# Performance work log

Hardware: AMD Instinct MI355X
Metric: run time of the kernel (lower is better)

## Reference

```python
import jax, jax.numpy as jnp
import numpy as np

B = 32768
N_SPARSE = 26
N_DENSE = 13
VOCAB = 10000
E = 64
H = 2
L = 3
DH = E // H
DNN_IN = N_DENSE + N_SPARSE * E  # 1677
H1, H2 = 256, 128


def setup_inputs() -> dict:
    key = jax.random.key(0)
    ks = jax.random.split(key, 12)
    sparse_idx = jax.random.randint(ks[0], (B, N_SPARSE), 0, VOCAB, dtype=jnp.int32)
    dense = jax.random.uniform(ks[1], (B, N_DENSE), dtype=jnp.float32)
    X = jnp.concatenate([sparse_idx.astype(jnp.float32), dense], axis=1)  # [B,39]
    emb_tables = jax.random.normal(ks[2], (N_SPARSE, VOCAB, E), dtype=jnp.float32)
    Wq = jax.random.normal(ks[3], (L, E, E), dtype=jnp.float32) * 0.05
    Wk = jax.random.normal(ks[4], (L, E, E), dtype=jnp.float32) * 0.05
    Wv = jax.random.normal(ks[5], (L, E, E), dtype=jnp.float32) * 0.05
    Wres = jax.random.normal(ks[6], (L, E, E), dtype=jnp.float32) * 0.05
    dnn_W1 = jax.random.normal(ks[7], (DNN_IN, H1), dtype=jnp.float32) * 1e-4
    dnn_b1 = jnp.zeros((H1,), dtype=jnp.float32)
    dnn_W2 = jax.random.normal(ks[8], (H1, H2), dtype=jnp.float32) * 1e-4
    dnn_b2 = jnp.zeros((H2,), dtype=jnp.float32)
    out_W = jax.random.normal(ks[9], (N_SPARSE * E + H2, 1), dtype=jnp.float32) * 1e-5
    lin_W = jax.random.normal(ks[10], (N_SPARSE + N_DENSE, 1), dtype=jnp.float32) * 1e-5
    lin_b = jnp.zeros((1,), dtype=jnp.float32)
    return {"X": X, "sparse_idx": sparse_idx, "emb_tables": emb_tables,
            "Wq": Wq, "Wk": Wk, "Wv": Wv, "Wres": Wres,
            "dnn_W1": dnn_W1, "dnn_b1": dnn_b1, "dnn_W2": dnn_W2, "dnn_b2": dnn_b2,
            "out_W": out_W, "lin_W": lin_W, "lin_b": lin_b}


def _split_heads(x):
    # torch.stack(torch.split(x, DH, dim=2)) -> [H, B, F, DH]
    b, f, _ = x.shape
    return jnp.moveaxis(x.reshape(b, f, H, DH), 2, 0)


def _interacting_layer(att, wq, wk, wv, wres):
    # att: [B, F, E]
    q = _split_heads(jnp.einsum('bfe,eo->bfo', att, wq))  # [H,B,F,DH]
    k = _split_heads(jnp.einsum('bfe,eo->bfo', att, wk))
    v = _split_heads(jnp.einsum('bfe,eo->bfo', att, wv))
    scores = jnp.einsum('hbik,hbjk->hbij', q, k)           # [H,B,F,F] (no scaling: default scaling=False)
    attn = jax.nn.softmax(scores, axis=-1)
    out = jnp.einsum('hbij,hbjd->hbid', attn, v)           # [H,B,F,DH]
    b, f = att.shape[0], att.shape[1]
    out = jnp.moveaxis(out, 0, 2).reshape(b, f, E)         # cat heads along last dim
    out = out + jnp.einsum('bfe,eo->bfo', att, wres)       # residual (use_res=True)
    return jax.nn.relu(out)


def reference(X, sparse_idx, emb_tables, Wq, Wk, Wv, Wres,
              dnn_W1, dnn_b1, dnn_W2, dnn_b2, out_W, lin_W, lin_b):
    # linear logit tower (dropout in eval mode -> identity)
    logit = jax.nn.relu(X @ lin_W + lin_b)                 # [B,1]
    # embedding gather: table f indexed by sparse_idx[:,f]
    emb = emb_tables[jnp.arange(N_SPARSE), sparse_idx]     # [B, F, E]
    att = emb
    for l in range(L):
        att = _interacting_layer(att, Wq[l], Wk[l], Wv[l], Wres[l])
    att_flat = att.reshape(att.shape[0], -1)               # [B, F*E]
    sparse_flat = emb.reshape(emb.shape[0], -1)            # [B, F*E]
    dense_input = X[:, N_SPARSE:]                          # [B, 13]
    dnn_in = jnp.concatenate([dense_input, sparse_flat], axis=1)
    h = jax.nn.relu(dnn_in @ dnn_W1 + dnn_b1)
    h = jax.nn.relu(h @ dnn_W2 + dnn_b2)
    stack = jnp.concatenate([att_flat, h], axis=-1)
    logit = logit + stack @ out_W
    return jax.nn.sigmoid(logit)
```

## Files before the change

kernel.cpp:

```cpp
#include <hip/hip_runtime.h>
#include <math.h>

#define BATCH 32768
#define NSP 26
#define NDN 13
#define VOC 10000
#define EDIM 64
#define NLAY 3
#define HID1 256
#define HID2 128
#define XW 39
#define KCH 27

typedef __fp16   fp16x2 __attribute__((ext_vector_type(2)));
typedef _Float16 half8  __attribute__((ext_vector_type(8)));
typedef float float4v   __attribute__((ext_vector_type(4)));

__device__ __forceinline__ unsigned pkh(float lo, float hi) {
    fp16x2 h = __builtin_amdgcn_cvt_pkrtz(lo, hi);
    return __builtin_bit_cast(unsigned, h);
}
__device__ __forceinline__ unsigned short f2h(float f) {
    return __builtin_bit_cast(unsigned short, (_Float16)f);
}
__device__ __forceinline__ float h2f(unsigned short h) {
    return (float)__builtin_bit_cast(_Float16, h);
}
__device__ __forceinline__ uint2 pkC(float4v c) {
    uint2 r; r.x = pkh(c[0], c[1]); r.y = pkh(c[2], c[3]); return r;
}
__device__ __forceinline__ void st4(unsigned short* p, float4v v) {
    *(uint2*)p = pkC(v);
}
__device__ __forceinline__ half8 cat(uint2 a, uint2 b) {
    union { unsigned u[4]; half8 h; } r;
    r.u[0] = a.x; r.u[1] = a.y; r.u[2] = b.x; r.u[3] = b.y;
    return r.h;
}

__global__ void k_pack(const float* __restrict__ Wq, const float* __restrict__ Wk,
                       const float* __restrict__ Wv, const float* __restrict__ Wr,
                       const float* __restrict__ W1, const float* __restrict__ W2,
                       unsigned short* __restrict__ pW,
                       unsigned short* __restrict__ pW1,
                       unsigned short* __restrict__ pW2) {
    int bid = blockIdx.x;
    if (bid < 192) {
        int tid = bid * 256 + threadIdx.x;
        int j    = tid & 7;
        int lane = (tid >> 3) & 63;
        int kt   = (tid >> 9) & 1;
        int nt   = (tid >> 10) & 3;
        int m    = (tid >> 12) & 3;
        int l    = tid >> 14;
        const float* W = (m == 0) ? Wq : (m == 1) ? Wk : (m == 2) ? Wv : Wr;
        int k = kt * 32 + ((lane >> 4) << 3) + j;
        int n = nt * 16 + (lane & 15);
        pW[tid] = f2h(W[l * EDIM * EDIM + k * EDIM + n]);
    } else if (bid < 1920) {
        int tid = (bid - 192) * 256 + threadIdx.x;
        int j    = tid & 7;
        int lane = (tid >> 3) & 63;
        int nt   = (tid >> 9) & 15;
        int rest = tid >> 13;
        int kt = rest & 1, c = rest >> 1;
        int kl = kt * 32 + ((lane >> 4) << 3) + j;
        int n  = nt * 16 + (lane & 15);
        int row;
        if (c < NSP) row = 13 + c * 64 + kl;
        else         row = (kl < NDN) ? kl : -1;
        pW1[tid] = (row >= 0) ? f2h(W1[(long)row * HID1 + n]) : (unsigned short)0;
    } else {
        int tid = (bid - 1920) * 256 + threadIdx.x;
        int j    = tid & 7;
        int lane = (tid >> 3) & 63;
        int nt   = (tid >> 9) & 7;
        int kc   = tid >> 12;
        int k = kc * 32 + ((lane >> 4) << 3) + j;
        int n = nt * 16 + (lane & 15);
        pW2[tid] = f2h(W2[(long)k * HID2 + n]);
    }
}

__global__ void k_lin(const float* __restrict__ X, const float* __restrict__ lw,
                      const float* __restrict__ lb, float* __restrict__ logit0) {
    int b = blockIdx.x * 256 + threadIdx.x;
    float s = lb[0];
    const float* xr = X + (long)b * XW;
#pragma unroll
    for (int i = 0; i < XW; i++) s = fmaf(xr[i], lw[i], s);
    logit0[b] = fmaxf(s, 0.f);
}

__global__ __launch_bounds__(256, 4) void k_interact(
    const int* __restrict__ sidx, const float* __restrict__ emb,
    const unsigned short* __restrict__ pW, const float* __restrict__ outW,
    float* __restrict__ p1)
{
    __shared__ __align__(16) unsigned short att_s[4][32 * 72];

    const int wid  = threadIdx.x >> 6;
    const int lane = threadIdx.x & 63;
    const int b    = blockIdx.x * 4 + wid;
    unsigned short* att = att_s[wid];

    const int quad = lane >> 4;
    const int c16  = lane & 15;
    const float4v zero4 = {0.f, 0.f, 0.f, 0.f};

#pragma unroll
    for (int f = 0; f < NSP; f++) {
        int idx = sidx[b * NSP + f];
        att[f * 72 + lane] = f2h(emb[((long)(f * VOC + idx)) * EDIM + lane]);
    }
#pragma unroll
    for (int r = NSP; r < 32; r++) att[r * 72 + lane] = 0;
    __threadfence_block();

    for (int l = 0; l < NLAY; l++) {
        half8 Fatt[2][2];
#pragma unroll
        for (int qt = 0; qt < 2; qt++)
#pragma unroll
            for (int kt = 0; kt < 2; kt++)
                Fatt[qt][kt] = *(const half8*)&att[(qt*16 + c16)*72 + kt*32 + quad*8];

        const unsigned short* wl = pW + l * 16384;
        uint2 qpk[4][2];
        uint2 kpk[4][2];
        uint2 vpk[2][4];
        uint2 rpk[4][2];

#pragma unroll
        for (int m = 0; m < 4; m++) {
            half8 Wf[4][2];
#pragma unroll
            for (int nt = 0; nt < 4; nt++)
#pragma unroll
                for (int kt = 0; kt < 2; kt++)
                    Wf[nt][kt] = *(const half8*)&wl[(m*8 + nt*2 + kt)*512 + lane*8];

            if (m == 2) {
#pragma unroll
                for (int qt = 0; qt < 2; qt++)
#pragma unroll
                    for (int dt = 0; dt < 4; dt++) {
                        float4v acc = __builtin_amdgcn_mfma_f32_16x16x32_f16(
                            Fatt[qt][0], Wf[dt][0], zero4, 0, 0, 0);
                        acc = __builtin_amdgcn_mfma_f32_16x16x32_f16(
                            Fatt[qt][1], Wf[dt][1], acc, 0, 0, 0);
                        vpk[qt][dt] = pkC(acc);
                    }
            } else {
#pragma unroll
                for (int dt = 0; dt < 4; dt++)
#pragma unroll
                    for (int qt = 0; qt < 2; qt++) {
                        float4v acc = __builtin_amdgcn_mfma_f32_16x16x32_f16(
                            Wf[dt][0], Fatt[qt][0], zero4, 0, 0, 0);
                        acc = __builtin_amdgcn_mfma_f32_16x16x32_f16(
                            Wf[dt][1], Fatt[qt][1], acc, 0, 0, 0);
                        if (m == 0)      qpk[dt][qt] = pkC(acc);
                        else if (m == 1) kpk[dt][qt] = pkC(acc);
                        else             rpk[dt][qt] = pkC(acc);
                    }
            }
        }

        uint2 Ppk[2][2][2];
#pragma unroll
        for (int h = 0; h < 2; h++)
#pragma unroll
            for (int nq = 0; nq < 2; nq++) {
                half8 Qc = cat(qpk[h*2][nq], qpk[h*2+1][nq]);
                float4v S0 = __builtin_amdgcn_mfma_f32_16x16x32_f16(
                    cat(kpk[h*2][0], kpk[h*2+1][0]), Qc, zero4, 0, 0, 0);
                float4v S1 = __builtin_amdgcn_mfma_f32_16x16x32_f16(
                    cat(kpk[h*2][1], kpk[h*2+1][1]), Qc, zero4, 0, 0, 0);
                float sv[8];
#pragma unroll
                for (int r = 0; r < 4; r++) {
                    sv[r]     = S0[r];
                    sv[4 + r] = (quad*4 + r >= 10) ? -1e30f : S1[r];
                }
                float mx = sv[0];
#pragma unroll
                for (int j = 1; j < 8; j++) mx = fmaxf(mx, sv[j]);
                mx = fmaxf(mx, __shfl_xor(mx, 16));
                mx = fmaxf(mx, __shfl_xor(mx, 32));
                float e[8], sum = 0.f;
#pragma unroll
                for (int j = 0; j < 8; j++) {
                    e[j] = (j >= 4 && quad*4 + (j-4) >= 10) ? 0.f : __expf(sv[j] - mx);
                    sum += e[j];
                }
                sum += __shfl_xor(sum, 16);
                sum += __shfl_xor(sum, 32);
                float inv = 1.f / sum;
                Ppk[h][0][nq].x = pkh(e[0]*inv, e[1]*inv);
                Ppk[h][0][nq].y = pkh(e[2]*inv, e[3]*inv);
                Ppk[h][1][nq].x = pkh(e[4]*inv, e[5]*inv);
                Ppk[h][1][nq].y = pkh(e[6]*inv, e[7]*inv);
            }

#pragma unroll
        for (int h = 0; h < 2; h++)
#pragma unroll
            for (int md = 0; md < 2; md++) {
                int dt = h*2 + md;
                half8 Vc = cat(vpk[0][dt], vpk[1][dt]);
#pragma unroll
                for (int nq = 0; nq < 2; nq++) {
                    float4v O = __builtin_amdgcn_mfma_f32_16x16x32_f16(
                        Vc, cat(Ppk[h][0][nq], Ppk[h][1][nq]), zero4, 0, 0, 0);
                    uint2 rp = rpk[dt][nq];
                    float4v o;
                    o[0] = fmaxf(O[0] + h2f((unsigned short)(rp.x & 0xFFFF)), 0.f);
                    o[1] = fmaxf(O[1] + h2f((unsigned short)(rp.x >> 16)),   0.f);
                    o[2] = fmaxf(O[2] + h2f((unsigned short)(rp.y & 0xFFFF)), 0.f);
                    o[3] = fmaxf(O[3] + h2f((unsigned short)(rp.y >> 16)),   0.f);
                    st4(&att[(nq*16 + c16)*72 + dt*16 + quad*4], o);
                }
            }
        __threadfence_block();
    }

    float s = 0.f;
#pragma unroll
    for (int f = 0; f < NSP; f++)
        s = fmaf(h2f(att[f*72 + lane]), outW[f*EDIM + lane], s);
#pragma unroll
    for (int off = 32; off > 0; off >>= 1) s += __shfl_down(s, off);
    if (lane == 0) p1[b] = s;
}

__global__ __launch_bounds__(256) void k_dnn(
    const float* __restrict__ X, const int* __restrict__ sidx,
    const float* __restrict__ emb, const unsigned short* __restrict__ pW1,
    const float* __restrict__ b1, const unsigned short* __restrict__ pW2,
    const float* __restrict__ b2, const float* __restrict__ outW,
    const float* __restrict__ logit0, const float* __restrict__ p1,
    float* __restrict__ out)
{
    __shared__ __align__(16) unsigned short smem[64 * 264];
    unsigned short* Abuf  = smem;
    unsigned short* h1buf = smem;
    unsigned short* h2buf = smem;

    const int t    = threadIdx.x;
    const int lane = t & 63;
    const int w    = t >> 6;
    const int quad = lane >> 4;
    const int c16  = lane & 15;
    const int bM   = blockIdx.x * 64;
    const int sr   = t >> 2;
    const int part = t & 3;

    float4v acc[4][4];
#pragma unroll
    for (int mt = 0; mt < 4; mt++)
#pragma unroll
        for (int nt = 0; nt < 4; nt++) acc[mt][nt] = (float4v){0.f, 0.f, 0.f, 0.f};

    for (int c = 0; c < KCH; c++) {
        if (c < NSP) {
            int idx = sidx[(bM + sr) * NSP + c];
            const float4* src = (const float4*)(emb + ((long)(c * VOC + idx)) * EDIM + part * 16);
            float4 a = src[0], bb = src[1], cc = src[2], dd = src[3];
            uint4 w0 = { pkh(a.x,a.y),   pkh(a.z,a.w),   pkh(bb.x,bb.y), pkh(bb.z,bb.w) };
            uint4 w1 = { pkh(cc.x,cc.y), pkh(cc.z,cc.w), pkh(dd.x,dd.y), pkh(dd.z,dd.w) };
            *(uint4*)&Abuf[sr * 72 + part * 16]     = w0;
            *(uint4*)&Abuf[sr * 72 + part * 16 + 8] = w1;
        } else {
            unsigned short v[16];
#pragma unroll
            for (int i = 0; i < 16; i++) {
                int j = part * 16 + i;
                v[i] = (j < NDN) ? f2h(X[(long)(bM + sr) * XW + NSP + j])
                                 : (unsigned short)0;
            }
            *(uint4*)&Abuf[sr * 72 + part * 16]     = *(uint4*)&v[0];
            *(uint4*)&Abuf[sr * 72 + part * 16 + 8] = *(uint4*)&v[8];
        }
        __syncthreads();

#pragma unroll
        for (int kt = 0; kt < 2; kt++) {
            half8 Bf[4], Af[4];
#pragma unroll
            for (int nt = 0; nt < 4; nt++)
                Bf[nt] = *(const half8*)&pW1[((long)((c*2 + kt)*16 + w*4 + nt) * 64 + lane) * 8];
#pragma unroll
            for (int mt = 0; mt < 4; mt++)
                Af[mt] = *(const half8*)&Abuf[(mt*16 + c16)*72 + kt*32 + quad*8];
#pragma unroll
            for (int mt = 0; mt < 4; mt++)
#pragma unroll
                for (int nt = 0; nt < 4; nt++)
                    acc[mt][nt] = __builtin_amdgcn_mfma_f32_16x16x32_f16(
                        Af[mt], Bf[nt], acc[mt][nt], 0, 0, 0);
        }
        __syncthreads();
    }

#pragma unroll
    for (int nt = 0; nt < 4; nt++) {
        int n = w * 64 + nt * 16 + c16;
        float bias = b1[n];
#pragma unroll
        for (int mt = 0; mt < 4; mt++)
#pragma unroll
            for (int reg = 0; reg < 4; reg++)
                h1buf[(mt * 16 + quad * 4 + reg) * 264 + n] =
                    f2h(fmaxf(acc[mt][nt][reg] + bias, 0.f));
    }
    __syncthreads();

    float4v acc2[4][2];
#pragma unroll
    for (int mt = 0; mt < 4; mt++)
#pragma unroll
        for (int n2 = 0; n2 < 2; n2++) acc2[mt][n2] = (float4v){0.f, 0.f, 0.f, 0.f};
#pragma unroll
    for (int kc2 = 0; kc2 < 8; kc2++) {
        half8 Bf2[2], Af2[4];
#pragma unroll
        for (int n2 = 0; n2 < 2; n2++)
            Bf2[n2] = *(const half8*)&pW2[((kc2 * 8 + w * 2 + n2) * 64 + lane) * 8];
#pragma unroll
        for (int mt = 0; mt < 4; mt++)
            Af2[mt] = *(const half8*)&h1buf[(mt * 16 + c16) * 264 + kc2 * 32 + quad * 8];
#pragma unroll
        for (int mt = 0; mt < 4; mt++)
#pragma unroll
            for (int n2 = 0; n2 < 2; n2++)
                acc2[mt][n2] = __builtin_amdgcn_mfma_f32_16x16x32_f16(
                    Af2[mt], Bf2[n2], acc2[mt][n2], 0, 0, 0);
    }
    __syncthreads();

#pragma unroll
    for (int n2 = 0; n2 < 2; n2++) {
        int n = w * 32 + n2 * 16 + c16;
        float bias = b2[n];
#pragma unroll
        for (int mt = 0; mt < 4; mt++)
#pragma unroll
            for (int reg = 0; reg < 4; reg++)
                h2buf[(mt * 16 + quad * 4 + reg) * 136 + n] =
                    f2h(fmaxf(acc2[mt][n2][reg] + bias, 0.f));
    }
    __syncthreads();

    if (t < 64) {
        const float* ow2 = outW + NSP * EDIM;
        float s = 0.f;
#pragma unroll
        for (int c8 = 0; c8 < 16; c8++) {
            half8 h = *(const half8*)&h2buf[t * 136 + c8 * 8];
#pragma unroll
            for (int j = 0; j < 8; j++)
                s = fmaf((float)h[j], ow2[c8 * 8 + j], s);
        }
        int bb = bM + t;
        float logit = logit0[bb] + p1[bb] + s;
        out[bb] = 1.f / (1.f + __expf(-logit));
    }
}

extern "C" void kernel_launch(void* const* d_in, const int* in_sizes, int n_in,
                              void* d_out, int out_size, void* d_ws, size_t ws_size,
                              hipStream_t stream) {
    const float* X    = (const float*)d_in[0];
    const int*   sidx = (const int*)d_in[1];
    const float* emb  = (const float*)d_in[2];
    const float* Wq   = (const float*)d_in[3];
    const float* Wk   = (const float*)d_in[4];
    const float* Wv   = (const float*)d_in[5];
    const float* Wres = (const float*)d_in[6];
    const float* W1   = (const float*)d_in[7];
    const float* b1   = (const float*)d_in[8];
    const float* W2   = (const float*)d_in[9];
    const float* b2   = (const float*)d_in[10];
    const float* outW = (const float*)d_in[11];
    const float* linW = (const float*)d_in[12];
    const float* linb = (const float*)d_in[13];
    float* out = (float*)d_out;

    float* logit0 = (float*)d_ws;
    float* p1     = logit0 + BATCH;
    unsigned short* pW  = (unsigned short*)(p1 + BATCH);
    unsigned short* pW1 = pW + 49152;
    unsigned short* pW2 = pW1 + 442368;

    k_pack<<<2048, 256, 0, stream>>>(Wq, Wk, Wv, Wres, W1, W2, pW, pW1, pW2);
    k_lin<<<BATCH / 256, 256, 0, stream>>>(X, linW, linb, logit0);
    k_interact<<<BATCH / 4, 256, 0, stream>>>(sidx, emb, pW, outW, p1);
    k_dnn<<<BATCH / 64, 256, 0, stream>>>(X, sidx, emb, pW1, b1, pW2, b2, outW,
                                          logit0, p1, out);
}
```

Before: 341.5 us.

## Load DNN embedding A-fragments directly from global, drop LDS staging and barriers

k_dnn now gathers each embedding row straight into MFMA A-fragment registers instead of staging the tile in shared memory with two barriers per K chunk. The block tile drops from 64 to 32 rows so twice as many blocks launch, and launch bounds now request 4 blocks per CU. The aim is to cut barrier stalls and LDS traffic in the gather-bound first GEMM and give more waves to hide memory latency. In exchange each pW1 fragment is reused across fewer rows, so weight reads from cache double, and global gather accesses become less coalesced.

```diff
diff --git a/kernel.cpp b/kernel.cpp
--- a/kernel.cpp
+++ b/kernel.cpp
@@ -10,7 +10,6 @@
 #define HID1 256
 #define HID2 128
 #define XW 39
-#define KCH 27
 
 typedef __fp16   fp16x2 __attribute__((ext_vector_type(2)));
 typedef _Float16 half8  __attribute__((ext_vector_type(8)));
@@ -36,6 +35,9 @@
     union { unsigned u[4]; half8 h; } r;
     r.u[0] = a.x; r.u[1] = a.y; r.u[2] = b.x; r.u[3] = b.y;
     return r.h;
+}
+__device__ __forceinline__ half8 h8(uint4 u) {
+    union { uint4 u; half8 h; } r; r.u = u; return r.h;
 }
 
 __global__ void k_pack(const float* __restrict__ Wq, const float* __restrict__ Wk,
@@ -234,7 +236,7 @@
     if (lane == 0) p1[b] = s;
 }
 
-__global__ __launch_bounds__(256) void k_dnn(
+__global__ __launch_bounds__(256, 4) void k_dnn(
     const float* __restrict__ X, const int* __restrict__ sidx,
     const float* __restrict__ emb, const unsigned short* __restrict__ pW1,
     const float* __restrict__ b1, const unsigned short* __restrict__ pW2,
@@ -242,65 +244,69 @@
     const float* __restrict__ logit0, const float* __restrict__ p1,
     float* __restrict__ out)
 {
-    __shared__ __align__(16) unsigned short smem[64 * 264];
-    unsigned short* Abuf  = smem;
-    unsigned short* h1buf = smem;
-    unsigned short* h2buf = smem;
+    __shared__ __align__(16) unsigned short h1buf[32 * 264];
+    __shared__ __align__(16) unsigned short h2buf[32 * 136];
 
     const int t    = threadIdx.x;
     const int lane = t & 63;
     const int w    = t >> 6;
     const int quad = lane >> 4;
     const int c16  = lane & 15;
-    const int bM   = blockIdx.x * 64;
-    const int sr   = t >> 2;
-    const int part = t & 3;
-
-    float4v acc[4][4];
-#pragma unroll
-    for (int mt = 0; mt < 4; mt++)
+    const int bM   = blockIdx.x * 32;
+
+    float4v acc[2][4];
+#pragma unroll
+    for (int mt = 0; mt < 2; mt++)
 #pragma unroll
         for (int nt = 0; nt < 4; nt++) acc[mt][nt] = (float4v){0.f, 0.f, 0.f, 0.f};
 
-    for (int c = 0; c < KCH; c++) {
-        if (c < NSP) {
-            int idx = sidx[(bM + sr) * NSP + c];
-            const float4* src = (const float4*)(emb + ((long)(c * VOC + idx)) * EDIM + part * 16);
-            float4 a = src[0], bb = src[1], cc = src[2], dd = src[3];
-            uint4 w0 = { pkh(a.x,a.y),   pkh(a.z,a.w),   pkh(bb.x,bb.y), pkh(bb.z,bb.w) };
-            uint4 w1 = { pkh(cc.x,cc.y), pkh(cc.z,cc.w), pkh(dd.x,dd.y), pkh(dd.z,dd.w) };
-            *(uint4*)&Abuf[sr * 72 + part * 16]     = w0;
-            *(uint4*)&Abuf[sr * 72 + part * 16 + 8] = w1;
-        } else {
-            unsigned short v[16];
-#pragma unroll
-            for (int i = 0; i < 16; i++) {
-                int j = part * 16 + i;
-                v[i] = (j < NDN) ? f2h(X[(long)(bM + sr) * XW + NSP + j])
-                                 : (unsigned short)0;
-            }
-            *(uint4*)&Abuf[sr * 72 + part * 16]     = *(uint4*)&v[0];
-            *(uint4*)&Abuf[sr * 72 + part * 16 + 8] = *(uint4*)&v[8];
-        }
-        __syncthreads();
-
+    for (int c = 0; c < NSP; c++) {
+        const float* r0 = emb + ((long)(c * VOC + sidx[(bM + c16) * NSP + c])) * EDIM;
+        const float* r1 = emb + ((long)(c * VOC + sidx[(bM + 16 + c16) * NSP + c])) * EDIM;
 #pragma unroll
         for (int kt = 0; kt < 2; kt++) {
-            half8 Bf[4], Af[4];
+            const int ko = kt * 32 + quad * 8;
+            float4 a0 = *(const float4*)(r0 + ko), a1 = *(const float4*)(r0 + ko + 4);
+            float4 b0 = *(const float4*)(r1 + ko), b1v = *(const float4*)(r1 + ko + 4);
+            half8 Af[2];
+            Af[0] = h8((uint4){ pkh(a0.x,a0.y), pkh(a0.z,a0.w), pkh(a1.x,a1.y), pkh(a1.z,a1.w) });
+            Af[1] = h8((uint4){ pkh(b0.x,b0.y), pkh(b0.z,b0.w), pkh(b1v.x,b1v.y), pkh(b1v.z,b1v.w) });
+            half8 Bf[4];
 #pragma unroll
             for (int nt = 0; nt < 4; nt++)
                 Bf[nt] = *(const half8*)&pW1[((long)((c*2 + kt)*16 + w*4 + nt) * 64 + lane) * 8];
 #pragma unroll
-            for (int mt = 0; mt < 4; mt++)
-                Af[mt] = *(const half8*)&Abuf[(mt*16 + c16)*72 + kt*32 + quad*8];
-#pragma unroll
-            for (int mt = 0; mt < 4; mt++)
+            for (int mt = 0; mt < 2; mt++)
 #pragma unroll
                 for (int nt = 0; nt < 4; nt++)
                     acc[mt][nt] = __builtin_amdgcn_mfma_f32_16x16x32_f16(
                         Af[mt], Bf[nt], acc[mt][nt], 0, 0, 0);
         }
-        __syncthreads();
+    }
+    {
+        half8 Af[2];
+#pragma unroll
+        for (int mt = 0; mt < 2; mt++) {
+            const long xr = (long)(bM + mt*16 + c16) * XW + NSP;
+            float v[8];
+#pragma unroll
+            for (int j = 0; j < 8; j++) {
+                int k = quad * 8 + j;
+                v[j] = (k < NDN) ? X[xr + k] : 0.f;
+            }
+            Af[mt] = h8((uint4){ pkh(v[0],v[1]), pkh(v[2],v[3]),
+                                 pkh(v[4],v[5]), pkh(v[6],v[7]) });
+        }
+        half8 Bf[4];
+#pragma unroll
+        for (int nt = 0; nt < 4; nt++)
+            Bf[nt] = *(const half8*)&pW1[((long)((NSP*2)*16 + w*4 + nt) * 64 + lane) * 8];
+#pragma unroll
+        for (int mt = 0; mt < 2; mt++)
+#pragma unroll
+            for (int nt = 0; nt < 4; nt++)
+                acc[mt][nt] = __builtin_amdgcn_mfma_f32_16x16x32_f16(
+                    Af[mt], Bf[nt], acc[mt][nt], 0, 0, 0);
     }
 
 #pragma unroll
@@ -308,7 +314,7 @@
         int n = w * 64 + nt * 16 + c16;
         float bias = b1[n];
 #pragma unroll
-        for (int mt = 0; mt < 4; mt++)
+        for (int mt = 0; mt < 2; mt++)
 #pragma unroll
             for (int reg = 0; reg < 4; reg++)
                 h1buf[(mt * 16 + quad * 4 + reg) * 264 + n] =
@@ -316,35 +322,34 @@
     }
     __syncthreads();
 
-    float4v acc2[4][2];
-#pragma unroll
-    for (int mt = 0; mt < 4; mt++)
+    float4v acc2[2][2];
+#pragma unroll
+    for (int mt = 0; mt < 2; mt++)
 #pragma unroll
         for (int n2 = 0; n2 < 2; n2++) acc2[mt][n2] = (float4v){0.f, 0.f, 0.f, 0.f};
 #pragma unroll
     for (int kc2 = 0; kc2 < 8; kc2++) {
-        half8 Bf2[2], Af2[4];
+        half8 Bf2[2], Af2[2];
 #pragma unroll
         for (int n2 = 0; n2 < 2; n2++)
             Bf2[n2] = *(const half8*)&pW2[((kc2 * 8 + w * 2 + n2) * 64 + lane) * 8];
 #pragma unroll
-        for (int mt = 0; mt < 4; mt++)
+        for (int mt = 0; mt < 2; mt++)
             Af2[mt] = *(const half8*)&h1buf[(mt * 16 + c16) * 264 + kc2 * 32 + quad * 8];
 #pragma unroll
-        for (int mt = 0; mt < 4; mt++)
+        for (int mt = 0; mt < 2; mt++)
 #pragma unroll
             for (int n2 = 0; n2 < 2; n2++)
                 acc2[mt][n2] = __builtin_amdgcn_mfma_f32_16x16x32_f16(
                     Af2[mt], Bf2[n2], acc2[mt][n2], 0, 0, 0);
     }
-    __syncthreads();
 
 #pragma unroll
     for (int n2 = 0; n2 < 2; n2++) {
         int n = w * 32 + n2 * 16 + c16;
         float bias = b2[n];
 #pragma unroll
-        for (int mt = 0; mt < 4; mt++)
+        for (int mt = 0; mt < 2; mt++)
 #pragma unroll
             for (int reg = 0; reg < 4; reg++)
                 h2buf[(mt * 16 + quad * 4 + reg) * 136 + n] =
@@ -352,7 +357,7 @@
     }
     __syncthreads();
 
-    if (t < 64) {
+    if (t < 32) {
         const float* ow2 = outW + NSP * EDIM;
         float s = 0.f;
 #pragma unroll
@@ -396,6 +401,6 @@
     k_pack<<<2048, 256, 0, stream>>>(Wq, Wk, Wv, Wres, W1, W2, pW, pW1, pW2);
     k_lin<<<BATCH / 256, 256, 0, stream>>>(X, linW, linb, logit0);
     k_interact<<<BATCH / 4, 256, 0, stream>>>(sidx, emb, pW, outW, p1);
-    k_dnn<<<BATCH / 64, 256, 0, stream>>>(X, sidx, emb, pW1, b1, pW2, b2, outW,
+    k_dnn<<<BATCH / 32, 256, 0, stream>>>(X, sidx, emb, pW1, b1, pW2, b2, outW,
                                           logit0, p1, out);
 }
```

Result: slower. 405.7 us (+18.8%).
